# Kernel optimization log

Measured on AMD Instinct MI355X. Metric: run time of the kernel, lower is better.

The kernel has to match this reference:

```python
import jax, jax.numpy as jnp
import numpy as np
from jax import lax

# PRPN (Parse-Read-Predict Network), eval mode (all dropout off, BatchNorm in eval
# with running stats mean=0/var=1, rmask=ones). Submodule math follows the upstream
# yikangshen/PRPN implementation vendored by jiant: ParsingNetwork (conv gate stack,
# hard hardtanh memory gates with cumprod over slots), ReadingNetwork (masked-softmax
# attention over nslots memory + LayerNorm LSTM cell, shift-append memory update),
# PredictNetwork (attention over prediction memory, res=0 -> Linear+BN+Tanh head).

T, B, V, D, H, S, L, NL = 192, 32, 50000, 384, 384, 15, 5, 2
RES = 0.1
G4 = 4 * H
BN_SC = np.float32(1.0 / np.sqrt(1.0 + 1e-5))   # eval BatchNorm with mean=0, var=1
INV_SQRT_H = np.float32(1.0 / np.sqrt(H))


def _layer_norm(x, g, b, eps=1e-6):
    # torch-style LayerNorm with unbiased std (x.std(-1))
    mu = jnp.mean(x, -1, keepdims=True)
    var = jnp.sum((x - mu) ** 2, -1, keepdims=True) / (x.shape[-1] - 1)
    return g * (x - mu) / (jnp.sqrt(var) + eps) + b


def _msoftmax(logits, gate, eps=1e-8):
    # blocks.softmax: exp-normalize then multiply by (soft) gate mask before sum
    e = jnp.exp(logits - jnp.max(logits, -1, keepdims=True)) * gate
    return e / (jnp.sum(e, -1, keepdims=True) + eps)


def _forward(input_ids, emb_w, pconv1_w, pconv1_b, pbn_g, pbn_b, pconv2_w, pconv2_b,
             r_wih, r_bih, r_whh, r_bhh, r_lnih_g, r_lnih_b, r_lnhh_g, r_lnhh_b,
             r_lnc_g, r_lnc_b, r_proj_w, r_proj_b,
             p_proj_w, p_proj_b, p_ffd_w, p_ffd_b, p_bn_g, p_bn_b):
    emb = emb_w[input_ids]                                        # (T,B,D)

    # ---- ParsingNetwork ----
    x = jnp.concatenate([jnp.zeros((L, B, D), emb.dtype), emb], 0)  # (T+L,B,D), zero history
    xc = jnp.transpose(x, (1, 2, 0))                              # (B,D,T+L)
    h1 = lax.conv_general_dilated(xc, pconv1_w, (1,), 'VALID',
                                  dimension_numbers=('NCH', 'OIH', 'NCH'))
    h1 = h1 + pconv1_b[None, :, None]
    h1 = jax.nn.relu(pbn_g[None, :, None] * h1 * BN_SC + pbn_b[None, :, None])  # (B,H,T)
    half = H // 2
    # Conv1d(nhid, 2, 1, groups=2): channel 0 from first half, channel 1 from second
    gate = jax.nn.sigmoid(jnp.einsum('bct,c->bt', h1[:, :half], pconv2_w[0]) + pconv2_b[0])
    gate_next = jax.nn.sigmoid(jnp.einsum('bct,c->bt', h1[:, half:], pconv2_w[1]) + pconv2_b[1])
    cum = jnp.concatenate([jnp.full((B, S), 1e9, gate.dtype), gate], 1)  # init cum_gate = +inf
    gate_hat = jnp.stack([cum[:, S - k:S - k + T] for k in range(S)], 2)  # (B,T,S)

    def mem_gate(g):  # hard gates: (hardtanh((g-ghat)/res*2+1)+1)/2, cumprod over slots
        u = (jnp.clip((g[:, :, None] - gate_hat) / RES * 2.0 + 1.0, -1.0, 1.0) + 1.0) * 0.5
        return jnp.cumprod(u, axis=2)

    mg = jnp.transpose(mem_gate(gate), (1, 0, 2))                 # (T,B,S)
    mgn = jnp.transpose(mem_gate(gate_next), (1, 0, 2))           # (T,B,S)

    # ---- per-timestep Read / Predict-attention loop ----
    def step(carry, xs):
        mem_h, mem_c, pmem = carry       # (NL,B,S,H),(NL,B,S,H),(B,S,H)
        e_t, mg_t, mgn_t = xs
        h = e_t
        nh, nc = [], []
        for j in range(NL):
            mh, mc = mem_h[j], mem_c[j]
            key_j = jnp.concatenate([h, mh[:, -1]], -1) @ r_proj_w[j].T + r_proj_b[j]
            att = _msoftmax(jnp.einsum('bsh,bh->bs', mh, key_j) * INV_SQRT_H, mg_t)
            sel_h = jnp.einsum('bs,bsh->bh', att, mh)
            sel_c = jnp.einsum('bs,bsh->bh', att, mc)
            gates = (_layer_norm(h @ r_wih[j].T + r_bih[j], r_lnih_g[j], r_lnih_b[j])
                     + _layer_norm(sel_h @ r_whh[j].T + r_bhh[j], r_lnhh_g[j], r_lnhh_b[j]))
            i_g, f_g, c_g, o_g = jnp.split(gates, 4, axis=-1)
            c_new = jax.nn.sigmoid(f_g) * sel_c + jax.nn.sigmoid(i_g) * jnp.tanh(c_g)
            h_new = jax.nn.sigmoid(o_g) * jnp.tanh(_layer_norm(c_new, r_lnc_g[j], r_lnc_b[j]))
            nh.append(jnp.concatenate([mh[:, 1:], h_new[:, None]], 1))
            nc.append(jnp.concatenate([mc[:, 1:], c_new[:, None]], 1))
            h = h_new
        pkey = jnp.concatenate([h, pmem[:, -1]], -1) @ p_proj_w.T + p_proj_b
        patt = _msoftmax(jnp.einsum('bsh,bh->bs', pmem, pkey) * INV_SQRT_H, mgn_t)
        sel = jnp.einsum('bs,bsh->bh', patt, pmem)
        pmem_new = jnp.concatenate([pmem[:, 1:], h[:, None]], 1)
        return (jnp.stack(nh), jnp.stack(nc), pmem_new), (h, sel)

    carry0 = (jnp.zeros((NL, B, S, H), emb.dtype),
              jnp.zeros((NL, B, S, H), emb.dtype),
              jnp.zeros((B, S, H), emb.dtype))
    _, (out_h, out_sel) = lax.scan(step, carry0, (emb, mg, mgn))

    # ---- PredictNetwork head (res=0): Linear(2H->D) + BN(eval) + Tanh ----
    flat = jnp.concatenate([out_h.reshape(T * B, H), out_sel.reshape(T * B, H)], -1)
    y = flat @ p_ffd_w.T + p_ffd_b
    y = jnp.tanh(p_bn_g * y * BN_SC + p_bn_b)
    return y.reshape(T, B, D)


def setup_inputs() -> dict:
    key = jax.random.key(0)
    ks = iter(jax.random.split(key, 16))

    def rn(shape, s=0.05):
        return jax.random.normal(next(ks), shape, dtype=jnp.float32) * s

    return {
        "input_ids": jax.random.randint(next(ks), (T, B), 0, V),
        "emb_w": rn((V, D), 0.01),
        "pconv1_w": rn((H, D, L + 1)),
        "pconv1_b": jnp.zeros((H,), jnp.float32),
        "pbn_g": jnp.ones((H,), jnp.float32),
        "pbn_b": jnp.zeros((H,), jnp.float32),
        "pconv2_w": rn((2, H // 2)),
        "pconv2_b": jnp.zeros((2,), jnp.float32),
        "r_wih": rn((NL, G4, D)),
        "r_bih": jnp.zeros((NL, G4), jnp.float32),
        "r_whh": rn((NL, G4, H)),
        "r_bhh": jnp.zeros((NL, G4), jnp.float32),
        "r_lnih_g": jnp.ones((NL, G4), jnp.float32),
        "r_lnih_b": jnp.zeros((NL, G4), jnp.float32),
        "r_lnhh_g": jnp.ones((NL, G4), jnp.float32),
        "r_lnhh_b": jnp.zeros((NL, G4), jnp.float32),
        "r_lnc_g": jnp.ones((NL, H), jnp.float32),
        "r_lnc_b": jnp.zeros((NL, H), jnp.float32),
        "r_proj_w": rn((NL, H, D + H)),
        "r_proj_b": jnp.zeros((NL, H), jnp.float32),
        "p_proj_w": rn((H, 2 * H)),
        "p_proj_b": jnp.zeros((H,), jnp.float32),
        "p_ffd_w": rn((D, 2 * H)),
        "p_ffd_b": jnp.zeros((D,), jnp.float32),
        "p_bn_g": jnp.ones((D,), jnp.float32),
        "p_bn_b": jnp.zeros((D,), jnp.float32),
    }


def reference(input_ids, emb_w, pconv1_w, pconv1_b, pbn_g, pbn_b, pconv2_w, pconv2_b,
              r_wih, r_bih, r_whh, r_bhh, r_lnih_g, r_lnih_b, r_lnhh_g, r_lnhh_b,
              r_lnc_g, r_lnc_b, r_proj_w, r_proj_b,
              p_proj_w, p_proj_b, p_ffd_w, p_ffd_b, p_bn_g, p_bn_b):
    out = _forward(input_ids, emb_w, pconv1_w, pconv1_b, pbn_g, pbn_b, pconv2_w, pconv2_b,
                   r_wih, r_bih, r_whh, r_bhh, r_lnih_g, r_lnih_b, r_lnhh_g, r_lnhh_b,
                   r_lnc_g, r_lnc_b, r_proj_w, r_proj_b,
                   p_proj_w, p_proj_b, p_ffd_w, p_ffd_b, p_bn_g, p_bn_b)
    mask = input_ids != 0
    return out, mask
```

## Files before the change

kernel.cpp:

```cpp
#include <hip/hip_runtime.h>


#define TT 192
#define TB 6144

constexpr size_t O_EMB    = 0;
constexpr size_t O_IH0LN  = 2359296;
constexpr size_t O_KEY0E  = 11796480;
constexpr size_t O_MG     = 14155776;
constexpr size_t O_MGN    = 14247936;
constexpr size_t O_H1     = 14340096;
constexpr size_t O_P0S    = 14340096;
constexpr size_t O_P1S    = 14389248;
constexpr size_t O_IH1RAW = 14438400;
constexpr size_t O_KEY1H  = 14536704;
constexpr size_t O_KEY0MH = 14561280;
constexpr size_t O_KEY1MH = 14573568;
constexpr size_t O_PKEYH  = 14585856;
constexpr size_t O_PKEYMH = 14610432;
constexpr size_t O_HNEW0  = 14635008;
constexpr size_t O_HNEW1  = 14647296;
constexpr size_t O_BAR    = 14671872;
constexpr size_t O_DEADEND= 14672896;
constexpr size_t O_GATEA  = 16699392;
constexpr size_t O_GATEB  = 16705536;
constexpr size_t O_OUTHS  = 16711680;
constexpr size_t O_MEMH0  = 21430272;
constexpr size_t O_MEMC0  = 21614592;
constexpr size_t O_MEMH1  = 21798912;
constexpr size_t O_MEMC1  = 21983232;
constexpr size_t O_PMEM   = 22167552;
constexpr size_t O_P0     = 22351872;
constexpr size_t O_P1     = 23089152;
constexpr size_t O_STATEEND = 23826432;

#define A_GRP   0
#define A_ROOT  128
#define A_GEN   144
#define B_GRP   160
#define B_ROOT  272
#define B_GEN   288
#define PRCNT   304

__device__ __forceinline__ float sigmoidf(float x) { return 1.f / (1.f + expf(-x)); }

__device__ __forceinline__ float ldx(const float* p) {
  return __hip_atomic_load(p, __ATOMIC_RELAXED, __HIP_MEMORY_SCOPE_AGENT);
}
__device__ __forceinline__ void stx(float* p, float v) {
  __hip_atomic_store(p, v, __ATOMIC_RELAXED, __HIP_MEMORY_SCOPE_AGENT);
}
__device__ __forceinline__ float2 ldx2(const float* p) {
  unsigned long long v = __hip_atomic_load((const unsigned long long*)p,
                                           __ATOMIC_RELAXED, __HIP_MEMORY_SCOPE_AGENT);
  return __builtin_bit_cast(float2, v);
}
__device__ __forceinline__ void stx2(float* p, float2 v) {
  __hip_atomic_store((unsigned long long*)p, __builtin_bit_cast(unsigned long long, v),
                     __ATOMIC_RELAXED, __HIP_MEMORY_SCOPE_AGENT);
}
__device__ __forceinline__ unsigned ldu(const unsigned* p) {
  return __hip_atomic_load(p, __ATOMIC_RELAXED, __HIP_MEMORY_SCOPE_AGENT);
}

constexpr float BN_SC = 0.9999950000374997f;
constexpr float INV_SQRT_H = 0.05103103630798288f;

__device__ __forceinline__ float blockSum(float v, float* red) {
#pragma unroll
  for (int off = 32; off > 0; off >>= 1) v += __shfl_down(v, off, 64);
  __syncthreads();
  if ((threadIdx.x & 63) == 0) red[threadIdx.x >> 6] = v;
  __syncthreads();
  return red[0] + red[1] + red[2] + red[3];
}

__device__ __forceinline__ float2 blockSum2(float a, float b, float* red) {
#pragma unroll
  for (int off = 32; off > 0; off >>= 1) {
    a += __shfl_down(a, off, 64);
    b += __shfl_down(b, off, 64);
  }
  __syncthreads();
  if ((threadIdx.x & 63) == 0) { int w = threadIdx.x >> 6; red[2 * w] = a; red[2 * w + 1] = b; }
  __syncthreads();
  return make_float2(red[0] + red[2] + red[4] + red[6],
                     red[1] + red[3] + red[5] + red[7]);
}

__global__ __launch_bounds__(256) void k_zero(float* p, int n) {
  int i = blockIdx.x * 256 + threadIdx.x;
  int stride = gridDim.x * 256;
  for (; i < n; i += stride) p[i] = 0.f;
}

__global__ __launch_bounds__(256) void k_emb(const int* ids, const float* emb_w,
                                             float* emb, float* out) {
  size_t idx = (size_t)blockIdx.x * 256 + threadIdx.x;
  size_t stride = (size_t)gridDim.x * 256;
  for (size_t i = idx; i < (size_t)TB * 384; i += stride) {
    size_t tb = i / 384, d = i - tb * 384;
    int id = ids[tb];
    emb[i] = emb_w[(size_t)id * 384 + d];
    if (i < TB) out[(size_t)TB * 384 + i] = (ids[i] != 0) ? 1.f : 0.f;
  }
}

__global__ __launch_bounds__(256) void k_conv(const float* emb, const float* W1, const float* cbias,
                                              const float* bng, const float* bnb, float* h1) {
  __shared__ float As[32][68];
  __shared__ float Bs[32][68];
  int n0 = blockIdx.x * 64, m0 = blockIdx.y * 64;
  int tid = threadIdx.x;
  float acc[4][4] = {};
  int mi = tid >> 3, kq = tid & 7;
  int ni = tid >> 2, kb = tid & 3;
  for (int kk = 0; kk < 2304; kk += 32) {
    int kc = kk / 384, dbase = kk - kc * 384;
    __syncthreads();
#pragma unroll
    for (int p = 0; p < 2; ++p) {
      int m = m0 + mi + 32 * p;
      int b = m / 192, t = m - b * 192;
      int tt = t + kc - 5;
      float4 v = {0.f, 0.f, 0.f, 0.f};
      if (tt >= 0) v = *(const float4*)(emb + ((size_t)tt * 32 + b) * 384 + dbase + kq * 4);
      As[kq * 4 + 0][mi + 32 * p] = v.x; As[kq * 4 + 1][mi + 32 * p] = v.y;
      As[kq * 4 + 2][mi + 32 * p] = v.z; As[kq * 4 + 3][mi + 32 * p] = v.w;
    }
#pragma unroll
    for (int i = 0; i < 8; ++i) {
      int d = dbase + kb * 8 + i;
      Bs[kb * 8 + i][ni] = W1[(size_t)(n0 + ni) * 2304 + d * 6 + kc];
    }
    __syncthreads();
    int ty = tid >> 4, tx = tid & 15;
#pragma unroll
    for (int k = 0; k < 32; ++k) {
      float4 a = *(const float4*)(&As[k][ty * 4]);
      float4 bv = *(const float4*)(&Bs[k][tx * 4]);
      acc[0][0] += a.x * bv.x; acc[0][1] += a.x * bv.y; acc[0][2] += a.x * bv.z; acc[0][3] += a.x * bv.w;
      acc[1][0] += a.y * bv.x; acc[1][1] += a.y * bv.y; acc[1][2] += a.y * bv.z; acc[1][3] += a.y * bv.w;
      acc[2][0] += a.z * bv.x; acc[2][1] += a.z * bv.y; acc[2][2] += a.z * bv.z; acc[2][3] += a.z * bv.w;
      acc[3][0] += a.w * bv.x; acc[3][1] += a.w * bv.y; acc[3][2] += a.w * bv.z; acc[3][3] += a.w * bv.w;
    }
  }
  int ty = tid >> 4, tx = tid & 15;
#pragma unroll
  for (int i = 0; i < 4; ++i) {
    int m = m0 + ty * 4 + i;
#pragma unroll
    for (int j = 0; j < 4; ++j) {
      int n = n0 + tx * 4 + j;
      float v = acc[i][j] + cbias[n];
      v = bng[n] * v * BN_SC + bnb[n];
      h1[(size_t)m * 384 + n] = fmaxf(v, 0.f);
    }
  }
}

__global__ __launch_bounds__(256) void k_gate(const float* h1, const float* w2, const float* b2,
                                              float* gA, float* gB) {
  __shared__ float red[8];
  int bt = blockIdx.x, tid = threadIdx.x;
  float v0 = 0.f, v1 = 0.f;
  if (tid < 192) {
    v0 = h1[(size_t)bt * 384 + tid] * w2[tid];
    v1 = h1[(size_t)bt * 384 + 192 + tid] * w2[192 + tid];
  }
  float s0 = blockSum(v0, red);
  float s1 = blockSum(v1, red);
  if (tid == 0) {
    gA[bt] = 1.f / (1.f + expf(-(s0 + b2[0])));
    gB[bt] = 1.f / (1.f + expf(-(s1 + b2[1])));
  }
}

__global__ __launch_bounds__(256) void k_mg(const float* gA, const float* gB, float* mg, float* mgn) {
  int idx = blockIdx.x * 256 + threadIdx.x;
  if (idx >= TB) return;
  int t = idx >> 5, b = idx & 31;
  float g = gA[b * 192 + t], gn = gB[b * 192 + t];
  float p = 1.f, pn = 1.f;
  for (int k = 0; k < 15; ++k) {
    float ghat = (k <= t) ? gA[b * 192 + t - k] : 1e9f;
    float u = fminf(fmaxf((g - ghat) / 0.1f * 2.f + 1.f, -1.f), 1.f);
    float un = fminf(fmaxf((gn - ghat) / 0.1f * 2.f + 1.f, -1.f), 1.f);
    p *= (u + 1.f) * 0.5f;
    pn *= (un + 1.f) * 0.5f;
    mg[(size_t)idx * 15 + k] = p;
    mgn[(size_t)idx * 15 + k] = pn;
  }
}

__global__ __launch_bounds__(256) void k_gemm(const float* A, int lda, const float* W, int ldw,
                                              const float* bias, float* Cf, int ldc, int K, int mode,
                                              const float* bng, const float* bnb, float* Cb) {
  __shared__ float As[32][68];
  __shared__ float Bs[32][68];
  int n0 = blockIdx.x * 64, m0 = blockIdx.y * 64;
  int tid = threadIdx.x;
  float acc[4][4] = {};
  int mi = tid >> 3, kq = tid & 7;
  int ni = tid >> 2, kb = tid & 3;
  for (int kk = 0; kk < K; kk += 32) {
    __syncthreads();
#pragma unroll
    for (int p = 0; p < 2; ++p) {
      int m = m0 + mi + 32 * p;
      float4 v = *(const float4*)(A + (size_t)m * lda + kk + kq * 4);
      As[kq * 4 + 0][mi + 32 * p] = v.x; As[kq * 4 + 1][mi + 32 * p] = v.y;
      As[kq * 4 + 2][mi + 32 * p] = v.z; As[kq * 4 + 3][mi + 32 * p] = v.w;
    }
    {
      const float* wp = W + (size_t)(n0 + ni) * ldw + kk + kb * 8;
      float4 q0 = *(const float4*)(wp);
      float4 q1 = *(const float4*)(wp + 4);
      Bs[kb * 8 + 0][ni] = q0.x; Bs[kb * 8 + 1][ni] = q0.y;
      Bs[kb * 8 + 2][ni] = q0.z; Bs[kb * 8 + 3][ni] = q0.w;
      Bs[kb * 8 + 4][ni] = q1.x; Bs[kb * 8 + 5][ni] = q1.y;
      Bs[kb * 8 + 6][ni] = q1.z; Bs[kb * 8 + 7][ni] = q1.w;
    }
    __syncthreads();
    int ty = tid >> 4, tx = tid & 15;
#pragma unroll
    for (int k = 0; k < 32; ++k) {
      float4 a = *(const float4*)(&As[k][ty * 4]);
      float4 bv = *(const float4*)(&Bs[k][tx * 4]);
      acc[0][0] += a.x * bv.x; acc[0][1] += a.x * bv.y; acc[0][2] += a.x * bv.z; acc[0][3] += a.x * bv.w;
      acc[1][0] += a.y * bv.x; acc[1][1] += a.y * bv.y; acc[1][2] += a.y * bv.z; acc[1][3] += a.y * bv.w;
      acc[2][0] += a.z * bv.x; acc[2][1] += a.z * bv.y; acc[2][2] += a.z * bv.z; acc[2][3] += a.z * bv.w;
      acc[3][0] += a.w * bv.x; acc[3][1] += a.w * bv.y; acc[3][2] += a.w * bv.z; acc[3][3] += a.w * bv.w;
    }
  }
  int ty = tid >> 4, tx = tid & 15;
#pragma unroll
  for (int i = 0; i < 4; ++i) {
    int m = m0 + ty * 4 + i;
#pragma unroll
    for (int j = 0; j < 4; ++j) {
      int n = n0 + tx * 4 + j;
      float v = acc[i][j];
      if (bias) v += bias[n];
      if (mode == 0) Cf[(size_t)m * ldc + n] = v;
      else Cb[(size_t)m * ldc + n] = tanhf(bng[n] * v * BN_SC + bnb[n]);
    }
  }
}

__global__ __launch_bounds__(256) void k_ln_rows(float* X, const float* g, const float* bt) {
  __shared__ float red[8];
  float* x = X + (size_t)blockIdx.x * 1536;
  int tid = threadIdx.x;
  float ps = 0.f;
  for (int i = tid; i < 1536; i += 256) ps += x[i];
  float mu = blockSum(ps, red) * (1.f / 1536.f);
  ps = 0.f;
  for (int i = tid; i < 1536; i += 256) { float d = x[i] - mu; ps += d * d; }
  float inv = 1.f / (sqrtf(blockSum(ps, red) * (1.f / 1535.f)) + 1e-6f);
  for (int i = tid; i < 1536; i += 256) x[i] = g[i] * (x[i] - mu) * inv + bt[i];
}

struct ScanArgs {
  float* ws;
  const float *r_whh, *r_bhh, *r_lnhh_g, *r_lnhh_b, *r_lnih_g, *r_lnih_b;
  const float *r_lnc_g, *r_lnc_b, *r_wih, *r_bih, *r_proj_w, *r_proj_b;
  const float *p_proj_w, *p_proj_b;
};

struct GJob { const float* W; int ldw; int koff; const float* bias; float* dst; int rstride; int ncols; };

__device__ __forceinline__ void resolveJob(const GJob* J, int col, const float*& W, int& ldw, int& koff,
                                           const float*& bias, float*& dst, int& rstride, int& cc) {
  int c = col;
#pragma unroll
  for (int j = 0; j < 4; ++j) {
    if (c < J[j].ncols) {
      W = J[j].W; ldw = J[j].ldw; koff = J[j].koff; bias = J[j].bias;
      dst = J[j].dst; rstride = J[j].rstride; cc = c; return;
    }
    c -= J[j].ncols;
  }
  W = J[0].W; ldw = J[0].ldw; koff = J[0].koff; bias = J[0].bias;
  dst = J[0].dst; rstride = J[0].rstride; cc = 0;
}

__device__ __forceinline__ void gate_arrive(unsigned* bar, int grpBase, int rootOff,
                                            int genOff, int g, int ngroups, unsigned k) {
  unsigned a = __hip_atomic_fetch_add(bar + grpBase + g * 16, 1u, __ATOMIC_RELAXED, __HIP_MEMORY_SCOPE_AGENT);
  if (a == k * 16u + 15u) {
    unsigned r = __hip_atomic_fetch_add(bar + rootOff, 1u, __ATOMIC_RELAXED, __HIP_MEMORY_SCOPE_AGENT);
    if (r == k * (unsigned)ngroups + (unsigned)(ngroups - 1))
      __hip_atomic_store(bar + genOff, k + 1u, __ATOMIC_RELAXED, __HIP_MEMORY_SCOPE_AGENT);
  }
}
__device__ __forceinline__ void waitgen(const unsigned* bar, int genOff, unsigned tgt) {
  while (ldu(bar + genOff) < tgt) __builtin_amdgcn_s_sleep(2);
}

__device__ __forceinline__ void stage_x(const float* src, float* xs) {
  const int tid = threadIdx.x;
  for (int j2 = tid; j2 < 6144; j2 += 256) {
    int j = j2 * 2;
    int bb = j / 384, kk = j - bb * 384;
    float2 v = ldx2(src + j);
    xs[bb * 385 + kk] = v.x; xs[bb * 385 + kk + 1] = v.y;
  }
}

__device__ void gemv_run(const GJob* J, int cbase, int ncols, const float* xs, float* red) {
  const int tid = threadIdx.x;
  const int b = tid & 31, cg = tid >> 5;
  float xr[48];
  const float* xp = xs + b * 385 + cg * 48;
#pragma unroll
  for (int q = 0; q < 48; ++q) xr[q] = xp[q];
  for (int ch = 0; ch < ncols; ch += 21) {
    const int nch = min(21, ncols - ch);
    for (int ci = 0; ci < nch; ++ci) {
      const float* W; int ldw, koff; const float* bias; float* dst; int rstride; int cc;
      resolveJob(J, cbase + ch + ci, W, ldw, koff, bias, dst, rstride, cc);
      const float* wr = W + (size_t)cc * ldw + koff + cg * 48;
      float a = 0.f;
#pragma unroll
      for (int q = 0; q < 12; ++q) {
        float4 w = *(const float4*)(wr + q * 4);
        a += w.x * xr[q * 4 + 0] + w.y * xr[q * 4 + 1]
           + w.z * xr[q * 4 + 2] + w.w * xr[q * 4 + 3];
      }
      a += __shfl_down(a, 32, 64);
      if ((cg & 1) == 0) red[((cg >> 1) * nch + ci) * 33 + b] = a;
    }
    __syncthreads();
    const int pairs = nch * 32;
    for (int pi = tid; pi < pairs; pi += 256) {
      int bb = pi / nch, ci = pi - bb * nch;
      float s = red[(0 * nch + ci) * 33 + bb] + red[(1 * nch + ci) * 33 + bb]
              + red[(2 * nch + ci) * 33 + bb] + red[(3 * nch + ci) * 33 + bb];
      const float* W; int ldw, koff; const float* bias; float* dst; int rstride; int cc;
      resolveJob(J, cbase + ch + ci, W, ldw, koff, bias, dst, rstride, cc);
      if (bias) s += bias[cc];
      stx(dst + (size_t)bb * rstride + cc, s);
    }
    __syncthreads();
  }
}

__device__ void preload_l0(int t, int b, const ScanArgs& A, float* sm) {
  float* ws = A.ws;
  const int tid = threadIdx.x;
  const size_t tb = (size_t)t * 32 + b;
  float* keyl = sm; float* gih = sm + 1984;
  for (int n = tid; n < 1536; n += 256) gih[n] = ws[O_IH0LN + tb * 1536 + n];
  if (tid < 192) {
    float2 v = *(const float2*)(ws + O_KEY0E + tb * 384 + 2 * tid);
    keyl[2 * tid] = v.x; keyl[2 * tid + 1] = v.y;
  }
}

__device__ void per_b_attn(int t, const float* memh, float* sm, const float* mgp) {
  const int tid = threadIdx.x;
  float* keyl = sm; float* logit = sm + 384; float* att = sm + 400;
  float mgv = (tid < 15) ? mgp[tid] : 0.f;
  __syncthreads();
  {
    int s = tid >> 4, l = tid & 15;
    if (s < 15) {
      const float* mh = memh + ((t + s) % 15) * 384;
      float p = 0.f;
      for (int k = l; k < 384; k += 16) p += mh[k] * keyl[k];
      p += __shfl_down(p, 8, 64); p += __shfl_down(p, 4, 64);
      p += __shfl_down(p, 2, 64); p += __shfl_down(p, 1, 64);
      if (l == 0) logit[s] = p * INV_SQRT_H;
    }
  }
  __syncthreads();
  if (tid < 64) {
    float lg = (tid < 15) ? logit[tid] : -3.0e38f;
    lg = fmaxf(lg, __shfl_xor(lg, 8, 64));
    lg = fmaxf(lg, __shfl_xor(lg, 4, 64));
    lg = fmaxf(lg, __shfl_xor(lg, 2, 64));
    lg = fmaxf(lg, __shfl_xor(lg, 1, 64));
    float e = (tid < 15) ? expf(logit[tid] - lg) * mgv : 0.f;
    float ssum = e;
    ssum += __shfl_xor(ssum, 1, 64); ssum += __shfl_xor(ssum, 2, 64);
    ssum += __shfl_xor(ssum, 4, 64); ssum += __shfl_xor(ssum, 8, 64);
    if (tid < 15) att[tid] = e / (ssum + 1e-8f);
  }
  __syncthreads();
}

__device__ void per_b_tail(int layer, int t, int b, const ScanArgs& A, float* sm,
                           float* memh, float* memc, const float* mir,
                           float mu_ih, float inv_ih) {
  float* ws = A.ws;
  const int tid = threadIdx.x;
  const size_t tb = (size_t)t * 32 + b;
  float* att = sm + 400; float* red = sm + 416;
  float* ghh = sm + 448; float* gih = sm + 1984; float* selc = sm + 3520;
  float* cnew = sm + 3904; float* ogat = sm + 4288;
  float av[15]; int pidx[15];
#pragma unroll
  for (int i = 0; i < 15; ++i) { av[i] = att[i]; pidx[i] = (t + i) % 15; }
  const float* bhh = A.r_bhh + layer * 1536;
  for (int n = tid; n < 1536; n += 256) {
    float acc = bhh[n];
#pragma unroll
    for (int i = 0; i < 15; ++i) acc += av[i] * mir[(size_t)pidx[i] * 1536 + n];
    ghh[n] = acc;
  }
  for (int h = tid; h < 384; h += 256) {
    float acc = 0.f;
#pragma unroll
    for (int i = 0; i < 15; ++i) acc += av[i] * memc[pidx[i] * 384 + h];
    selc[h] = acc;
  }
  __syncthreads();
  float s1 = 0.f, s2 = 0.f;
  for (int n = tid; n < 1536; n += 256) { float v = ghh[n]; s1 += v; s2 += v * v; }
  float2 rhh = blockSum2(s1, s2, red);
  float mu_hh = rhh.x * (1.f / 1536.f);
  float inv_hh = 1.f / (sqrtf(fmaxf(rhh.y - rhh.x * mu_hh, 0.f) * (1.f / 1535.f)) + 1e-6f);
  const float *hg = A.r_lnhh_g + layer * 1536, *hb = A.r_lnhh_b + layer * 1536;
  const float *ig = A.r_lnih_g + 1536, *ib = A.r_lnih_b + 1536;
  for (int h = tid; h < 384; h += 256) {
    float gi, gf, gc, go;
    if (layer == 0) {
      gi = gih[h]; gf = gih[384 + h]; gc = gih[768 + h]; go = gih[1152 + h];
    } else {
      gi = ig[h] * (gih[h] - mu_ih) * inv_ih + ib[h];
      gf = ig[384 + h] * (gih[384 + h] - mu_ih) * inv_ih + ib[384 + h];
      gc = ig[768 + h] * (gih[768 + h] - mu_ih) * inv_ih + ib[768 + h];
      go = ig[1152 + h] * (gih[1152 + h] - mu_ih) * inv_ih + ib[1152 + h];
    }
    gi += hg[h] * (ghh[h] - mu_hh) * inv_hh + hb[h];
    gf += hg[384 + h] * (ghh[384 + h] - mu_hh) * inv_hh + hb[384 + h];
    gc += hg[768 + h] * (ghh[768 + h] - mu_hh) * inv_hh + hb[768 + h];
    go += hg[1152 + h] * (ghh[1152 + h] - mu_hh) * inv_hh + hb[1152 + h];
    float c = sigmoidf(gf) * selc[h] + sigmoidf(gi) * tanhf(gc);
    cnew[h] = c; ogat[h] = go;
  }
  __syncthreads();
  s1 = 0.f; s2 = 0.f;
  for (int h = tid; h < 384; h += 256) { float v = cnew[h]; s1 += v; s2 += v * v; }
  float2 rc = blockSum2(s1, s2, red);
  float mu_c = rc.x * (1.f / 384.f);
  float inv_c = 1.f / (sqrtf(fmaxf(rc.y - rc.x * mu_c, 0.f) * (1.f / 383.f)) + 1e-6f);
  const float *lcg = A.r_lnc_g + layer * 384, *lcb = A.r_lnc_b + layer * 384;
  const int slot = t % 15;
  if (tid < 192) {
    int h0 = 2 * tid, h1 = h0 + 1;
    float c0 = cnew[h0], c1 = cnew[h1];
    float hn0 = sigmoidf(ogat[h0]) * tanhf(lcg[h0] * (c0 - mu_c) * inv_c + lcb[h0]);
    float hn1 = sigmoidf(ogat[h1]) * tanhf(lcg[h1] * (c1 - mu_c) * inv_c + lcb[h1]);
    *(float2*)(memh + slot * 384 + h0) = make_float2(hn0, hn1);
    *(float2*)(memc + slot * 384 + h0) = make_float2(c0, c1);
    if (layer == 0) {
      stx2(ws + O_HNEW0 + (size_t)b * 384 + h0, make_float2(hn0, hn1));
    } else {
      stx2(ws + O_HNEW1 + (size_t)(t & 1) * 12288 + (size_t)b * 384 + h0, make_float2(hn0, hn1));
      *(float2*)(ws + O_OUTHS + tb * 768 + h0) = make_float2(hn0, hn1);
    }
  }
}

__device__ void per_b_layer0(int t, int b, const ScanArgs& A, float* sm) {
  float* ws = A.ws;
  const int tid = threadIdx.x;
  const size_t tb = (size_t)t * 32 + b;
  float* memh = ws + O_MEMH0 + (size_t)b * 5760;
  float* memc = ws + O_MEMC0 + (size_t)b * 5760;
  float* mir  = ws + O_P0 + (size_t)b * 23040;
  const float* stg = ws + O_P0S + (size_t)b * 1536;
  float* keyl = sm;
  const int pslot = (t + 14) % 15;
#pragma unroll
  for (int i = 0; i < 3; ++i) {
    int idx = tid + i * 256;
    float2 v = ldx2(stg + 2 * idx);
    *(float2*)(mir + (size_t)pslot * 1536 + 2 * idx) = v;
  }
  if (tid < 192) {
    float2 c = ldx2(ws + O_KEY0MH + (size_t)b * 384 + 2 * tid);
    keyl[2 * tid] += c.x; keyl[2 * tid + 1] += c.y;
  }
  per_b_attn(t, memh, sm, ws + O_MG + tb * 15);
  per_b_tail(0, t, b, A, sm, memh, memc, mir, 0.f, 0.f);
}

__device__ void per_b_layer1(int t, int b, const ScanArgs& A, float* sm) {
  float* ws = A.ws;
  const int tid = threadIdx.x;
  const size_t tb = (size_t)t * 32 + b;
  const size_t par = (size_t)(t & 1);
  float* memh = ws + O_MEMH1 + (size_t)b * 5760;
  float* memc = ws + O_MEMC1 + (size_t)b * 5760;
  float* mir  = ws + O_P1 + (size_t)b * 23040;
  const float* stg = ws + O_P1S + (size_t)b * 1536;
  float* keyl = sm; float* red = sm + 416; float* gih = sm + 1984;
  const int pslot = (t + 14) % 15;
#pragma unroll
  for (int i = 0; i < 3; ++i) {
    int idx = tid + i * 256;
    float2 v = ldx2(stg + 2 * idx);
    *(float2*)(mir + (size_t)pslot * 1536 + 2 * idx) = v;
  }
#pragma unroll
  for (int i = 0; i < 3; ++i) {
    int idx = tid + i * 256;
    float2 v = ldx2(ws + O_IH1RAW + par * 49152 + (size_t)b * 1536 + 2 * idx);
    gih[2 * idx] = v.x; gih[2 * idx + 1] = v.y;
  }
  if (tid < 192) {
    float2 a = ldx2(ws + O_KEY1H + par * 12288 + (size_t)b * 384 + 2 * tid);
    float2 c = ldx2(ws + O_KEY1MH + (size_t)b * 384 + 2 * tid);
    keyl[2 * tid] = a.x + c.x; keyl[2 * tid + 1] = a.y + c.y;
  }
  per_b_attn(t, memh, sm, ws + O_MG + tb * 15);
  float s1 = 0.f, s2 = 0.f;
  for (int n = tid; n < 1536; n += 256) { float v = gih[n]; s1 += v; s2 += v * v; }
  float2 rih = blockSum2(s1, s2, red);
  float mu_ih = rih.x * (1.f / 1536.f);
  float inv_ih = 1.f / (sqrtf(fmaxf(rih.y - rih.x * mu_ih, 0.f) * (1.f / 1535.f)) + 1e-6f);
  per_b_tail(1, t, b, A, sm, memh, memc, mir, mu_ih, inv_ih);
}

__device__ void per_b_predict(int t, int b, const ScanArgs& A, float* sm) {
  float* ws = A.ws;
  const int tid = threadIdx.x;
  const size_t tb = (size_t)t * 32 + b;
  float* pmem = ws + O_PMEM + (size_t)b * 5760;
  float* keyl = sm; float* logit = sm + 384; float* att = sm + 400;
  if (tid < 192) {
    float2 a = ldx2(ws + O_PKEYH + (size_t)(t & 1) * 12288 + (size_t)b * 384 + 2 * tid);
    float2 c = ldx2(ws + O_PKEYMH + (size_t)((t + 1) & 1) * 12288 + (size_t)b * 384 + 2 * tid);
    keyl[2 * tid] = a.x + c.x; keyl[2 * tid + 1] = a.y + c.y;
  }
  float mgv = (tid < 15) ? ws[O_MGN + tb * 15 + tid] : 0.f;
  __syncthreads();
  {
    int s = tid >> 4, l = tid & 15;
    if (s < 15) {
      const float* mh = pmem + ((t + s) % 15) * 384;
      float p = 0.f;
      for (int k = l; k < 384; k += 16) p += mh[k] * keyl[k];
      p += __shfl_down(p, 8, 64); p += __shfl_down(p, 4, 64);
      p += __shfl_down(p, 2, 64); p += __shfl_down(p, 1, 64);
      if (l == 0) logit[s] = p * INV_SQRT_H;
    }
  }
  __syncthreads();
  if (tid < 64) {
    float lg = (tid < 15) ? logit[tid] : -3.0e38f;
    lg = fmaxf(lg, __shfl_xor(lg, 8, 64));
    lg = fmaxf(lg, __shfl_xor(lg, 4, 64));
    lg = fmaxf(lg, __shfl_xor(lg, 2, 64));
    lg = fmaxf(lg, __shfl_xor(lg, 1, 64));
    float e = (tid < 15) ? expf(logit[tid] - lg) * mgv : 0.f;
    float ssum = e;
    ssum += __shfl_xor(ssum, 1, 64); ssum += __shfl_xor(ssum, 2, 64);
    ssum += __shfl_xor(ssum, 4, 64); ssum += __shfl_xor(ssum, 8, 64);
    if (tid < 15) att[tid] = e / (ssum + 1e-8f);
  }
  __syncthreads();
  float av[15]; int pidx[15];
#pragma unroll
  for (int i = 0; i < 15; ++i) { av[i] = att[i]; pidx[i] = (t + i) % 15; }
  for (int h = tid; h < 384; h += 256) {
    float acc = 0.f;
#pragma unroll
    for (int i = 0; i < 15; ++i) acc += av[i] * pmem[pidx[i] * 384 + h];
    ws[O_OUTHS + tb * 768 + 384 + h] = acc;
  }
  __syncthreads();
  if (tid < 192) {
    const int slot = t % 15;
    float2 v = ldx2(ws + O_HNEW1 + (size_t)(t & 1) * 12288 + (size_t)b * 384 + 2 * tid);
    *(float2*)(pmem + slot * 384 + 2 * tid) = v;
  }
}

__global__ __launch_bounds__(256) void k_scan(ScanArgs A) {
  __shared__ float sm[15104];
  float* ws = A.ws;
  unsigned* bar = (unsigned*)(ws + O_BAR);
  const int wg = blockIdx.x;
  const int tid = threadIdx.x;

  if (wg < 32) {
    const int b = wg, g = wg >> 4;
    preload_l0(0, b, A, sm);
    __syncthreads();
    unsigned ka = 0;
    for (int t = 0; t < 192; ++t, ka += 2) {
      per_b_layer0(t, b, A, sm);
      __syncthreads();
      if (tid == 0) gate_arrive(bar, A_GRP, A_ROOT, A_GEN, g, 8, ka);
      if (t + 1 < 192) preload_l0(t + 1, b, A, sm);
      __syncthreads();
      if (tid == 0) {
        waitgen(bar, A_GEN, ka + 1);
        gate_arrive(bar, A_GRP, A_ROOT, A_GEN, g, 8, ka + 1);
        waitgen(bar, A_GEN, ka + 2);
      }
      __syncthreads();
    }
  } else if (wg < 128) {
    const int g = wg >> 4;
    const int cbase = (wg - 32) * 40;
    float* xs = sm; float* red = sm + 12320;
    unsigned ka = 0;
    for (int t = 0; t < 192; ++t, ka += 2) {
      if (tid == 0) {
        gate_arrive(bar, A_GRP, A_ROOT, A_GEN, g, 8, ka);
        waitgen(bar, A_GEN, ka + 1);
      }
      __syncthreads();
      stage_x(ws + O_HNEW0, xs);
      if (tid == 0 && t >= 2) waitgen(bar, B_GEN, 2u * t - 3u);
      __syncthreads();
      {
        const size_t par = (size_t)(t & 1);
        GJob J[4] = {
          { A.r_wih + 589824, 384, 0, A.r_bih + 1536, ws + O_IH1RAW + par * 49152, 1536, 1536 },
          { A.r_proj_w + 294912, 768, 0, A.r_proj_b + 384, ws + O_KEY1H + par * 12288, 384, 384 },
          { A.r_whh, 384, 0, nullptr, ws + O_P0S, 1536, 1536 },
          { A.r_proj_w, 768, 384, nullptr, ws + O_KEY0MH, 384, 384 },
        };
        gemv_run(J, cbase, 40, xs, red);
      }
      if (tid == 0) {
        gate_arrive(bar, A_GRP, A_ROOT, A_GEN, g, 8, ka + 1);
        waitgen(bar, A_GEN, ka + 2);
      }
      __syncthreads();
    }
  } else if (wg < 160) {
    const int b = wg - 128, g = (wg - 128) >> 4;
    unsigned kb = 0;
    for (int t = 0; t < 192; ++t, kb += 2) {
      if (tid == 0) waitgen(bar, A_GEN, 2u * t + 2u);
      __syncthreads();
      per_b_layer1(t, b, A, sm);
      __syncthreads();
      if (tid == 0) {
        gate_arrive(bar, B_GRP, B_ROOT, B_GEN, g, 6, kb);
        waitgen(bar, B_GEN, kb + 1);
        gate_arrive(bar, B_GRP, B_ROOT, B_GEN, g, 6, kb + 1);
        waitgen(bar, B_GEN, kb + 2);
      }
      __syncthreads();
    }
  } else if (wg < 224) {
    const int g = (wg - 128) >> 4;
    const int cbase = (wg - 160) * 42;
    float* xs = sm; float* red = sm + 12320;
    unsigned kb = 0;
    for (int t = 0; t < 192; ++t, kb += 2) {
      if (tid == 0) {
        gate_arrive(bar, B_GRP, B_ROOT, B_GEN, g, 6, kb);
        waitgen(bar, B_GEN, kb + 1);
      }
      __syncthreads();
      stage_x(ws + O_HNEW1 + (size_t)(t & 1) * 12288, xs);
      if (tid == 0) {
        while (ldu(bar + PRCNT) < 32u * (unsigned)t) __builtin_amdgcn_s_sleep(2);
      }
      __syncthreads();
      {
        const size_t par = (size_t)(t & 1);
        GJob J[4] = {
          { A.r_whh + 589824, 384, 0, nullptr, ws + O_P1S, 1536, 1536 },
          { A.r_proj_w + 294912, 768, 384, nullptr, ws + O_KEY1MH, 384, 384 },
          { A.p_proj_w, 768, 0, A.p_proj_b, ws + O_PKEYH + par * 12288, 384, 384 },
          { A.p_proj_w, 768, 384, nullptr, ws + O_PKEYMH + par * 12288, 384, 384 },
        };
        gemv_run(J, cbase, 42, xs, red);
      }
      if (tid == 0) {
        gate_arrive(bar, B_GRP, B_ROOT, B_GEN, g, 6, kb + 1);
        waitgen(bar, B_GEN, kb + 2);
      }
      __syncthreads();
    }
  } else {
    const int b = wg - 224;
    for (int t = 0; t < 192; ++t) {
      if (tid == 0) waitgen(bar, B_GEN, 2u * t + 2u);
      __syncthreads();
      per_b_predict(t, b, A, sm);
      __syncthreads();
      if (tid == 0)
        __hip_atomic_fetch_add(bar + PRCNT, 1u, __ATOMIC_RELAXED, __HIP_MEMORY_SCOPE_AGENT);
    }
  }
}

extern "C" void kernel_launch(void* const* d_in, const int* in_sizes, int n_in,
                              void* d_out, int out_size, void* d_ws, size_t ws_size,
                              hipStream_t stream) {
  const int* ids = (const int*)d_in[0];
  const float* emb_w = (const float*)d_in[1];
  const float* pconv1_w = (const float*)d_in[2];
  const float* pconv1_b = (const float*)d_in[3];
  const float* pbn_g = (const float*)d_in[4];
  const float* pbn_b = (const float*)d_in[5];
  const float* pconv2_w = (const float*)d_in[6];
  const float* pconv2_b = (const float*)d_in[7];
  const float* r_wih = (const float*)d_in[8];
  const float* r_bih = (const float*)d_in[9];
  const float* r_whh = (const float*)d_in[10];
  const float* r_bhh = (const float*)d_in[11];
  const float* r_lnih_g = (const float*)d_in[12];
  const float* r_lnih_b = (const float*)d_in[13];
  const float* r_lnhh_g = (const float*)d_in[14];
  const float* r_lnhh_b = (const float*)d_in[15];
  const float* r_lnc_g = (const float*)d_in[16];
  const float* r_lnc_b = (const float*)d_in[17];
  const float* r_proj_w = (const float*)d_in[18];
  const float* r_proj_b = (const float*)d_in[19];
  const float* p_proj_w = (const float*)d_in[20];
  const float* p_proj_b = (const float*)d_in[21];
  const float* p_ffd_w = (const float*)d_in[22];
  const float* p_ffd_b = (const float*)d_in[23];
  const float* p_bn_g = (const float*)d_in[24];
  const float* p_bn_b = (const float*)d_in[25];
  float* ws = (float*)d_ws;
  float* out = (float*)d_out;

  k_zero<<<1024, 256, 0, stream>>>(ws + O_MEMH0, (int)(O_STATEEND - O_MEMH0));
  k_emb<<<4096, 256, 0, stream>>>(ids, emb_w, ws + O_EMB, out);
  k_conv<<<dim3(6, 96), 256, 0, stream>>>(ws + O_EMB, pconv1_w, pconv1_b, pbn_g, pbn_b, ws + O_H1);
  k_gate<<<6144, 256, 0, stream>>>(ws + O_H1, pconv2_w, pconv2_b, ws + O_GATEA, ws + O_GATEB);
  k_mg<<<24, 256, 0, stream>>>(ws + O_GATEA, ws + O_GATEB, ws + O_MG, ws + O_MGN);
  k_zero<<<326, 256, 0, stream>>>(ws + O_P0S, (int)(O_DEADEND - O_P0S));
  k_gemm<<<dim3(24, 96), 256, 0, stream>>>(ws + O_EMB, 384, r_wih, 384, r_bih,
                                           ws + O_IH0LN, 1536, 384, 0, nullptr, nullptr, nullptr);
  k_gemm<<<dim3(6, 96), 256, 0, stream>>>(ws + O_EMB, 384, r_proj_w, 768, r_proj_b,
                                          ws + O_KEY0E, 384, 384, 0, nullptr, nullptr, nullptr);
  k_ln_rows<<<6144, 256, 0, stream>>>(ws + O_IH0LN, r_lnih_g, r_lnih_b);
  ScanArgs SA{ws, r_whh, r_bhh, r_lnhh_g, r_lnhh_b, r_lnih_g, r_lnih_b,
              r_lnc_g, r_lnc_b, r_wih, r_bih, r_proj_w, r_proj_b, p_proj_w, p_proj_b};
  k_scan<<<256, 256, 0, stream>>>(SA);
  k_gemm<<<dim3(6, 96), 256, 0, stream>>>(ws + O_OUTHS, 768, p_ffd_w, 768, p_ffd_b,
                                          nullptr, 384, 768, 1, p_bn_g, p_bn_b, out);
}
```

Before: 13.15 ms.

## Replace grouped barriers with per-block progress flags and wave-per-batch recurrent cells

The persistent scan kernel's hierarchical generation barriers give way to per-workgroup monotonic progress flags. Each consumer polls only the producers it depends on, so layer 0, layer 1, predict and the GEMV groups can run skewed in a pipeline instead of in lockstep. The per-batch cell work (attention, LayerNorm-LSTM, predict) moves from a full 256-thread block per batch element to one wave per batch element, using register-resident data and wave shuffles instead of block-wide syncs. The grid shrinks from 256 to 184 blocks. The risks are subtle ordering bugs under relaxed atomics and lower parallelism per batch step.

```diff
diff --git a/kernel.cpp b/kernel.cpp
--- a/kernel.cpp
+++ b/kernel.cpp
@@ -21,7 +21,7 @@
 constexpr size_t O_HNEW0  = 14635008;
 constexpr size_t O_HNEW1  = 14647296;
 constexpr size_t O_BAR    = 14671872;
-constexpr size_t O_DEADEND= 14672896;
+constexpr size_t O_DEADEND= 14675968;
 constexpr size_t O_GATEA  = 16699392;
 constexpr size_t O_GATEB  = 16705536;
 constexpr size_t O_OUTHS  = 16711680;
@@ -34,13 +34,11 @@
 constexpr size_t O_P1     = 23089152;
 constexpr size_t O_STATEEND = 23826432;
 
-#define A_GRP   0
-#define A_ROOT  128
-#define A_GEN   144
-#define B_GRP   160
-#define B_ROOT  272
-#define B_GEN   288
-#define PRCNT   304
+#define L0F 0
+#define L1F 512
+#define PRF 1024
+#define G0F 1536
+#define G1F 3072
 
 __device__ __forceinline__ float sigmoidf(float x) { return 1.f / (1.f + expf(-x)); }
 
@@ -59,8 +57,11 @@
   __hip_atomic_store((unsigned long long*)p, __builtin_bit_cast(unsigned long long, v),
                      __ATOMIC_RELAXED, __HIP_MEMORY_SCOPE_AGENT);
 }
-__device__ __forceinline__ unsigned ldu(const unsigned* p) {
+__device__ __forceinline__ int ldi(const int* p) {
   return __hip_atomic_load(p, __ATOMIC_RELAXED, __HIP_MEMORY_SCOPE_AGENT);
+}
+__device__ __forceinline__ void sti(int* p, int v) {
+  __hip_atomic_store(p, v, __ATOMIC_RELAXED, __HIP_MEMORY_SCOPE_AGENT);
 }
 
 constexpr float BN_SC = 0.9999950000374997f;
@@ -75,17 +76,13 @@
   return red[0] + red[1] + red[2] + red[3];
 }
 
-__device__ __forceinline__ float2 blockSum2(float a, float b, float* red) {
+__device__ __forceinline__ float2 wred2(float a, float b) {
 #pragma unroll
   for (int off = 32; off > 0; off >>= 1) {
-    a += __shfl_down(a, off, 64);
-    b += __shfl_down(b, off, 64);
-  }
-  __syncthreads();
-  if ((threadIdx.x & 63) == 0) { int w = threadIdx.x >> 6; red[2 * w] = a; red[2 * w + 1] = b; }
-  __syncthreads();
-  return make_float2(red[0] + red[2] + red[4] + red[6],
-                     red[1] + red[3] + red[5] + red[7]);
+    a += __shfl_xor(a, off, 64);
+    b += __shfl_xor(b, off, 64);
+  }
+  return make_float2(a, b);
 }
 
 __global__ __launch_bounds__(256) void k_zero(float* p, int n) {
@@ -285,19 +282,6 @@
   dst = J[0].dst; rstride = J[0].rstride; cc = 0;
 }
 
-__device__ __forceinline__ void gate_arrive(unsigned* bar, int grpBase, int rootOff,
-                                            int genOff, int g, int ngroups, unsigned k) {
-  unsigned a = __hip_atomic_fetch_add(bar + grpBase + g * 16, 1u, __ATOMIC_RELAXED, __HIP_MEMORY_SCOPE_AGENT);
-  if (a == k * 16u + 15u) {
-    unsigned r = __hip_atomic_fetch_add(bar + rootOff, 1u, __ATOMIC_RELAXED, __HIP_MEMORY_SCOPE_AGENT);
-    if (r == k * (unsigned)ngroups + (unsigned)(ngroups - 1))
-      __hip_atomic_store(bar + genOff, k + 1u, __ATOMIC_RELAXED, __HIP_MEMORY_SCOPE_AGENT);
-  }
-}
-__device__ __forceinline__ void waitgen(const unsigned* bar, int genOff, unsigned tgt) {
-  while (ldu(bar + genOff) < tgt) __builtin_amdgcn_s_sleep(2);
-}
-
 __device__ __forceinline__ void stage_x(const float* src, float* xs) {
   const int tid = threadIdx.x;
   for (int j2 = tid; j2 < 6144; j2 += 256) {
@@ -346,354 +330,418 @@
   }
 }
 
-__device__ void preload_l0(int t, int b, const ScanArgs& A, float* sm) {
+__device__ __forceinline__ void wave_attn(const float* memh, const float* klds, const float* mgp,
+                                          int t, int lane, float (&att)[15]) {
+  const int g = lane >> 2, l = lane & 3;
+  float part = 0.f;
+  if (g < 15) {
+    const float* mh = memh + ((t + g) % 15) * 384 + l;
+#pragma unroll 8
+    for (int k = 0; k < 96; ++k) part += mh[4 * k] * klds[l + 4 * k];
+  }
+  part += __shfl_xor(part, 1, 64);
+  part += __shfl_xor(part, 2, 64);
+  float logit[15];
+#pragma unroll
+  for (int s = 0; s < 15; ++s) logit[s] = __shfl(part, 4 * s, 64) * INV_SQRT_H;
+  float m = logit[0];
+#pragma unroll
+  for (int s = 1; s < 15; ++s) m = fmaxf(m, logit[s]);
+  float sum = 0.f;
+#pragma unroll
+  for (int s = 0; s < 15; ++s) { att[s] = expf(logit[s] - m) * mgp[s]; sum += att[s]; }
+  float inv = 1.f / (sum + 1e-8f);
+#pragma unroll
+  for (int s = 0; s < 15; ++s) att[s] *= inv;
+}
+
+__device__ void l0_loop(int b, int lane, float* klds, const ScanArgs& A, int* bar) {
   float* ws = A.ws;
-  const int tid = threadIdx.x;
-  const size_t tb = (size_t)t * 32 + b;
-  float* keyl = sm; float* gih = sm + 1984;
-  for (int n = tid; n < 1536; n += 256) gih[n] = ws[O_IH0LN + tb * 1536 + n];
-  if (tid < 192) {
-    float2 v = *(const float2*)(ws + O_KEY0E + tb * 384 + 2 * tid);
-    keyl[2 * tid] = v.x; keyl[2 * tid + 1] = v.y;
-  }
-}
-
-__device__ void per_b_attn(int t, const float* memh, float* sm, const float* mgp) {
-  const int tid = threadIdx.x;
-  float* keyl = sm; float* logit = sm + 384; float* att = sm + 400;
-  float mgv = (tid < 15) ? mgp[tid] : 0.f;
-  __syncthreads();
-  {
-    int s = tid >> 4, l = tid & 15;
-    if (s < 15) {
-      const float* mh = memh + ((t + s) % 15) * 384;
-      float p = 0.f;
-      for (int k = l; k < 384; k += 16) p += mh[k] * keyl[k];
-      p += __shfl_down(p, 8, 64); p += __shfl_down(p, 4, 64);
-      p += __shfl_down(p, 2, 64); p += __shfl_down(p, 1, 64);
-      if (l == 0) logit[s] = p * INV_SQRT_H;
-    }
-  }
-  __syncthreads();
-  if (tid < 64) {
-    float lg = (tid < 15) ? logit[tid] : -3.0e38f;
-    lg = fmaxf(lg, __shfl_xor(lg, 8, 64));
-    lg = fmaxf(lg, __shfl_xor(lg, 4, 64));
-    lg = fmaxf(lg, __shfl_xor(lg, 2, 64));
-    lg = fmaxf(lg, __shfl_xor(lg, 1, 64));
-    float e = (tid < 15) ? expf(logit[tid] - lg) * mgv : 0.f;
-    float ssum = e;
-    ssum += __shfl_xor(ssum, 1, 64); ssum += __shfl_xor(ssum, 2, 64);
-    ssum += __shfl_xor(ssum, 4, 64); ssum += __shfl_xor(ssum, 8, 64);
-    if (tid < 15) att[tid] = e / (ssum + 1e-8f);
-  }
-  __syncthreads();
-}
-
-__device__ void per_b_tail(int layer, int t, int b, const ScanArgs& A, float* sm,
-                           float* memh, float* memc, const float* mir,
-                           float mu_ih, float inv_ih) {
-  float* ws = A.ws;
-  const int tid = threadIdx.x;
-  const size_t tb = (size_t)t * 32 + b;
-  float* att = sm + 400; float* red = sm + 416;
-  float* ghh = sm + 448; float* gih = sm + 1984; float* selc = sm + 3520;
-  float* cnew = sm + 3904; float* ogat = sm + 4288;
-  float av[15]; int pidx[15];
-#pragma unroll
-  for (int i = 0; i < 15; ++i) { av[i] = att[i]; pidx[i] = (t + i) % 15; }
-  const float* bhh = A.r_bhh + layer * 1536;
-  for (int n = tid; n < 1536; n += 256) {
-    float acc = bhh[n];
-#pragma unroll
-    for (int i = 0; i < 15; ++i) acc += av[i] * mir[(size_t)pidx[i] * 1536 + n];
-    ghh[n] = acc;
-  }
-  for (int h = tid; h < 384; h += 256) {
-    float acc = 0.f;
-#pragma unroll
-    for (int i = 0; i < 15; ++i) acc += av[i] * memc[pidx[i] * 384 + h];
-    selc[h] = acc;
-  }
-  __syncthreads();
-  float s1 = 0.f, s2 = 0.f;
-  for (int n = tid; n < 1536; n += 256) { float v = ghh[n]; s1 += v; s2 += v * v; }
-  float2 rhh = blockSum2(s1, s2, red);
-  float mu_hh = rhh.x * (1.f / 1536.f);
-  float inv_hh = 1.f / (sqrtf(fmaxf(rhh.y - rhh.x * mu_hh, 0.f) * (1.f / 1535.f)) + 1e-6f);
-  const float *hg = A.r_lnhh_g + layer * 1536, *hb = A.r_lnhh_b + layer * 1536;
-  const float *ig = A.r_lnih_g + 1536, *ib = A.r_lnih_b + 1536;
-  for (int h = tid; h < 384; h += 256) {
-    float gi, gf, gc, go;
-    if (layer == 0) {
-      gi = gih[h]; gf = gih[384 + h]; gc = gih[768 + h]; go = gih[1152 + h];
-    } else {
-      gi = ig[h] * (gih[h] - mu_ih) * inv_ih + ib[h];
-      gf = ig[384 + h] * (gih[384 + h] - mu_ih) * inv_ih + ib[384 + h];
-      gc = ig[768 + h] * (gih[768 + h] - mu_ih) * inv_ih + ib[768 + h];
-      go = ig[1152 + h] * (gih[1152 + h] - mu_ih) * inv_ih + ib[1152 + h];
-    }
-    gi += hg[h] * (ghh[h] - mu_hh) * inv_hh + hb[h];
-    gf += hg[384 + h] * (ghh[384 + h] - mu_hh) * inv_hh + hb[384 + h];
-    gc += hg[768 + h] * (ghh[768 + h] - mu_hh) * inv_hh + hb[768 + h];
-    go += hg[1152 + h] * (ghh[1152 + h] - mu_hh) * inv_hh + hb[1152 + h];
-    float c = sigmoidf(gf) * selc[h] + sigmoidf(gi) * tanhf(gc);
-    cnew[h] = c; ogat[h] = go;
-  }
-  __syncthreads();
-  s1 = 0.f; s2 = 0.f;
-  for (int h = tid; h < 384; h += 256) { float v = cnew[h]; s1 += v; s2 += v * v; }
-  float2 rc = blockSum2(s1, s2, red);
-  float mu_c = rc.x * (1.f / 384.f);
-  float inv_c = 1.f / (sqrtf(fmaxf(rc.y - rc.x * mu_c, 0.f) * (1.f / 383.f)) + 1e-6f);
-  const float *lcg = A.r_lnc_g + layer * 384, *lcb = A.r_lnc_b + layer * 384;
-  const int slot = t % 15;
-  if (tid < 192) {
-    int h0 = 2 * tid, h1 = h0 + 1;
-    float c0 = cnew[h0], c1 = cnew[h1];
-    float hn0 = sigmoidf(ogat[h0]) * tanhf(lcg[h0] * (c0 - mu_c) * inv_c + lcb[h0]);
-    float hn1 = sigmoidf(ogat[h1]) * tanhf(lcg[h1] * (c1 - mu_c) * inv_c + lcb[h1]);
-    *(float2*)(memh + slot * 384 + h0) = make_float2(hn0, hn1);
-    *(float2*)(memc + slot * 384 + h0) = make_float2(c0, c1);
-    if (layer == 0) {
-      stx2(ws + O_HNEW0 + (size_t)b * 384 + h0, make_float2(hn0, hn1));
-    } else {
-      stx2(ws + O_HNEW1 + (size_t)(t & 1) * 12288 + (size_t)b * 384 + h0, make_float2(hn0, hn1));
-      *(float2*)(ws + O_OUTHS + tb * 768 + h0) = make_float2(hn0, hn1);
-    }
-  }
-}
-
-__device__ void per_b_layer0(int t, int b, const ScanArgs& A, float* sm) {
-  float* ws = A.ws;
-  const int tid = threadIdx.x;
-  const size_t tb = (size_t)t * 32 + b;
   float* memh = ws + O_MEMH0 + (size_t)b * 5760;
   float* memc = ws + O_MEMC0 + (size_t)b * 5760;
   float* mir  = ws + O_P0 + (size_t)b * 23040;
   const float* stg = ws + O_P0S + (size_t)b * 1536;
-  float* keyl = sm;
-  const int pslot = (t + 14) % 15;
-#pragma unroll
-  for (int i = 0; i < 3; ++i) {
-    int idx = tid + i * 256;
-    float2 v = ldx2(stg + 2 * idx);
-    *(float2*)(mir + (size_t)pslot * 1536 + 2 * idx) = v;
-  }
-  if (tid < 192) {
-    float2 c = ldx2(ws + O_KEY0MH + (size_t)b * 384 + 2 * tid);
-    keyl[2 * tid] += c.x; keyl[2 * tid + 1] += c.y;
-  }
-  per_b_attn(t, memh, sm, ws + O_MG + tb * 15);
-  per_b_tail(0, t, b, A, sm, memh, memc, mir, 0.f, 0.f);
-}
-
-__device__ void per_b_layer1(int t, int b, const ScanArgs& A, float* sm) {
+  const int* p1 = bar + G0F + lane * 16;
+  const int* p2 = bar + G0F + (64 + (lane & 31)) * 16;
+  for (int t = 0; t < 192; ++t) {
+    const size_t tb = (size_t)t * 32 + b;
+    float2 ih[12];
+#pragma unroll
+    for (int j = 0; j < 12; ++j)
+      ih[j] = *(const float2*)(ws + O_IH0LN + tb * 1536 + 2 * lane + 128 * j);
+    float2 kE[3];
+#pragma unroll
+    for (int j = 0; j < 3; ++j)
+      kE[j] = *(const float2*)(ws + O_KEY0E + tb * 384 + 2 * lane + 128 * j);
+    while (true) {
+      int a = ldi(p1);
+      int c = (lane < 32) ? ldi(p2) : 0x7fffffff;
+      if (__all(a >= t && c >= t)) break;
+      __builtin_amdgcn_s_sleep(1);
+    }
+    float2 fresh[12];
+#pragma unroll
+    for (int j = 0; j < 12; ++j) fresh[j] = ldx2(stg + 2 * lane + 128 * j);
+#pragma unroll
+    for (int j = 0; j < 3; ++j) {
+      float2 c2 = ldx2(ws + O_KEY0MH + (size_t)b * 384 + 2 * lane + 128 * j);
+      *(float2*)(klds + 2 * lane + 128 * j) = make_float2(kE[j].x + c2.x, kE[j].y + c2.y);
+    }
+    float att[15];
+    wave_attn(memh, klds, ws + O_MG + tb * 15, t, lane, att);
+    float2 acc[12];
+#pragma unroll
+    for (int j = 0; j < 12; ++j) {
+      float2 bb = *(const float2*)(A.r_bhh + 2 * lane + 128 * j);
+      acc[j] = make_float2(bb.x + att[14] * fresh[j].x, bb.y + att[14] * fresh[j].y);
+    }
+#pragma unroll
+    for (int s = 0; s < 14; ++s) {
+      const float* P = mir + ((t + s) % 15) * 1536;
+      float a = att[s];
+#pragma unroll
+      for (int j = 0; j < 12; ++j) {
+        float2 p = *(const float2*)(P + 2 * lane + 128 * j);
+        acc[j].x += a * p.x; acc[j].y += a * p.y;
+      }
+    }
+    float2 selc[3];
+#pragma unroll
+    for (int j = 0; j < 3; ++j) selc[j] = make_float2(0.f, 0.f);
+#pragma unroll
+    for (int s = 0; s < 15; ++s) {
+      const float* C = memc + ((t + s) % 15) * 384;
+      float a = att[s];
+#pragma unroll
+      for (int j = 0; j < 3; ++j) {
+        float2 p = *(const float2*)(C + 2 * lane + 128 * j);
+        selc[j].x += a * p.x; selc[j].y += a * p.y;
+      }
+    }
+    float s1 = 0.f, s2 = 0.f;
+#pragma unroll
+    for (int j = 0; j < 12; ++j) {
+      s1 += acc[j].x + acc[j].y;
+      s2 += acc[j].x * acc[j].x + acc[j].y * acc[j].y;
+    }
+    float2 r = wred2(s1, s2);
+    float mu = r.x * (1.f / 1536.f);
+    float inv = 1.f / (sqrtf(fmaxf(r.y - r.x * mu, 0.f) * (1.f / 1535.f)) + 1e-6f);
+    const float* hg = A.r_lnhh_g;
+    const float* hb = A.r_lnhh_b;
+    float2 cn[3], og[3];
+#pragma unroll
+    for (int jj = 0; jj < 3; ++jj) {
+      const int d = 2 * lane + 128 * jj;
+      float2 gi, gf, gc, go;
+      { float2 g2 = *(const float2*)(hg + d), b2 = *(const float2*)(hb + d);
+        gi.x = ih[jj].x + g2.x * (acc[jj].x - mu) * inv + b2.x;
+        gi.y = ih[jj].y + g2.y * (acc[jj].y - mu) * inv + b2.y; }
+      { float2 g2 = *(const float2*)(hg + 384 + d), b2 = *(const float2*)(hb + 384 + d);
+        gf.x = ih[3 + jj].x + g2.x * (acc[3 + jj].x - mu) * inv + b2.x;
+        gf.y = ih[3 + jj].y + g2.y * (acc[3 + jj].y - mu) * inv + b2.y; }
+      { float2 g2 = *(const float2*)(hg + 768 + d), b2 = *(const float2*)(hb + 768 + d);
+        gc.x = ih[6 + jj].x + g2.x * (acc[6 + jj].x - mu) * inv + b2.x;
+        gc.y = ih[6 + jj].y + g2.y * (acc[6 + jj].y - mu) * inv + b2.y; }
+      { float2 g2 = *(const float2*)(hg + 1152 + d), b2 = *(const float2*)(hb + 1152 + d);
+        go.x = ih[9 + jj].x + g2.x * (acc[9 + jj].x - mu) * inv + b2.x;
+        go.y = ih[9 + jj].y + g2.y * (acc[9 + jj].y - mu) * inv + b2.y; }
+      cn[jj].x = sigmoidf(gf.x) * selc[jj].x + sigmoidf(gi.x) * tanhf(gc.x);
+      cn[jj].y = sigmoidf(gf.y) * selc[jj].y + sigmoidf(gi.y) * tanhf(gc.y);
+      og[jj] = go;
+    }
+    s1 = 0.f; s2 = 0.f;
+#pragma unroll
+    for (int jj = 0; jj < 3; ++jj) {
+      s1 += cn[jj].x + cn[jj].y;
+      s2 += cn[jj].x * cn[jj].x + cn[jj].y * cn[jj].y;
+    }
+    r = wred2(s1, s2);
+    float mu_c = r.x * (1.f / 384.f);
+    float inv_c = 1.f / (sqrtf(fmaxf(r.y - r.x * mu_c, 0.f) * (1.f / 383.f)) + 1e-6f);
+    const int slot = t % 15;
+    const int pslot = (t + 14) % 15;
+#pragma unroll
+    for (int jj = 0; jj < 3; ++jj) {
+      const int d = 2 * lane + 128 * jj;
+      float2 lg2 = *(const float2*)(A.r_lnc_g + d), lb2 = *(const float2*)(A.r_lnc_b + d);
+      float2 hn;
+      hn.x = sigmoidf(og[jj].x) * tanhf(lg2.x * (cn[jj].x - mu_c) * inv_c + lb2.x);
+      hn.y = sigmoidf(og[jj].y) * tanhf(lg2.y * (cn[jj].y - mu_c) * inv_c + lb2.y);
+      *(float2*)(memh + slot * 384 + d) = hn;
+      *(float2*)(memc + slot * 384 + d) = cn[jj];
+      stx2(ws + O_HNEW0 + (size_t)b * 384 + d, hn);
+    }
+#pragma unroll
+    for (int j = 0; j < 12; ++j)
+      *(float2*)(mir + pslot * 1536 + 2 * lane + 128 * j) = fresh[j];
+    asm volatile("s_waitcnt vmcnt(0)" ::: "memory");
+    if (lane == 0) sti(bar + L0F + b * 16, t + 1);
+  }
+}
+
+__device__ void l1_loop(int b, int lane, float* klds, const ScanArgs& A, int* bar) {
   float* ws = A.ws;
-  const int tid = threadIdx.x;
-  const size_t tb = (size_t)t * 32 + b;
-  const size_t par = (size_t)(t & 1);
   float* memh = ws + O_MEMH1 + (size_t)b * 5760;
   float* memc = ws + O_MEMC1 + (size_t)b * 5760;
   float* mir  = ws + O_P1 + (size_t)b * 23040;
   const float* stg = ws + O_P1S + (size_t)b * 1536;
-  float* keyl = sm; float* red = sm + 416; float* gih = sm + 1984;
-  const int pslot = (t + 14) % 15;
-#pragma unroll
-  for (int i = 0; i < 3; ++i) {
-    int idx = tid + i * 256;
-    float2 v = ldx2(stg + 2 * idx);
-    *(float2*)(mir + (size_t)pslot * 1536 + 2 * idx) = v;
-  }
-#pragma unroll
-  for (int i = 0; i < 3; ++i) {
-    int idx = tid + i * 256;
-    float2 v = ldx2(ws + O_IH1RAW + par * 49152 + (size_t)b * 1536 + 2 * idx);
-    gih[2 * idx] = v.x; gih[2 * idx + 1] = v.y;
-  }
-  if (tid < 192) {
-    float2 a = ldx2(ws + O_KEY1H + par * 12288 + (size_t)b * 384 + 2 * tid);
-    float2 c = ldx2(ws + O_KEY1MH + (size_t)b * 384 + 2 * tid);
-    keyl[2 * tid] = a.x + c.x; keyl[2 * tid + 1] = a.y + c.y;
-  }
-  per_b_attn(t, memh, sm, ws + O_MG + tb * 15);
-  float s1 = 0.f, s2 = 0.f;
-  for (int n = tid; n < 1536; n += 256) { float v = gih[n]; s1 += v; s2 += v * v; }
-  float2 rih = blockSum2(s1, s2, red);
-  float mu_ih = rih.x * (1.f / 1536.f);
-  float inv_ih = 1.f / (sqrtf(fmaxf(rih.y - rih.x * mu_ih, 0.f) * (1.f / 1535.f)) + 1e-6f);
-  per_b_tail(1, t, b, A, sm, memh, memc, mir, mu_ih, inv_ih);
-}
-
-__device__ void per_b_predict(int t, int b, const ScanArgs& A, float* sm) {
+  const float* hg = A.r_lnhh_g + 1536;
+  const float* hb = A.r_lnhh_b + 1536;
+  const float* igp = A.r_lnih_g + 1536;
+  const float* ibp = A.r_lnih_b + 1536;
+  const float* bhh = A.r_bhh + 1536;
+  const float* lcg = A.r_lnc_g + 384;
+  const float* lcb = A.r_lnc_b + 384;
+  const int* p1 = bar + G0F + lane * 16;
+  const int* p2 = bar + G0F + (64 + (lane & 31)) * 16;
+  const int* p3 = bar + G1F + lane * 16;
+  for (int t = 0; t < 192; ++t) {
+    while (true) {
+      int a = ldi(p1);
+      int c = (lane < 32) ? ldi(p2) : 0x7fffffff;
+      int d2 = ldi(p3);
+      if (__all(a >= t + 1 && c >= t + 1 && d2 >= t)) break;
+      __builtin_amdgcn_s_sleep(1);
+    }
+    const size_t tb = (size_t)t * 32 + b;
+    const size_t par = (size_t)(t & 1);
+    float2 gx[12], fresh[12];
+#pragma unroll
+    for (int j = 0; j < 12; ++j) {
+      gx[j] = ldx2(ws + O_IH1RAW + par * 49152 + (size_t)b * 1536 + 2 * lane + 128 * j);
+      fresh[j] = ldx2(stg + 2 * lane + 128 * j);
+    }
+#pragma unroll
+    for (int j = 0; j < 3; ++j) {
+      float2 a2 = ldx2(ws + O_KEY1H + par * 12288 + (size_t)b * 384 + 2 * lane + 128 * j);
+      float2 c2 = ldx2(ws + O_KEY1MH + (size_t)b * 384 + 2 * lane + 128 * j);
+      *(float2*)(klds + 2 * lane + 128 * j) = make_float2(a2.x + c2.x, a2.y + c2.y);
+    }
+    float att[15];
+    wave_attn(memh, klds, ws + O_MG + tb * 15, t, lane, att);
+    float2 acc[12];
+#pragma unroll
+    for (int j = 0; j < 12; ++j) {
+      float2 bb = *(const float2*)(bhh + 2 * lane + 128 * j);
+      acc[j] = make_float2(bb.x + att[14] * fresh[j].x, bb.y + att[14] * fresh[j].y);
+    }
+#pragma unroll
+    for (int s = 0; s < 14; ++s) {
+      const float* P = mir + ((t + s) % 15) * 1536;
+      float a = att[s];
+#pragma unroll
+      for (int j = 0; j < 12; ++j) {
+        float2 p = *(const float2*)(P + 2 * lane + 128 * j);
+        acc[j].x += a * p.x; acc[j].y += a * p.y;
+      }
+    }
+    float2 selc[3];
+#pragma unroll
+    for (int j = 0; j < 3; ++j) selc[j] = make_float2(0.f, 0.f);
+#pragma unroll
+    for (int s = 0; s < 15; ++s) {
+      const float* C = memc + ((t + s) % 15) * 384;
+      float a = att[s];
+#pragma unroll
+      for (int j = 0; j < 3; ++j) {
+        float2 p = *(const float2*)(C + 2 * lane + 128 * j);
+        selc[j].x += a * p.x; selc[j].y += a * p.y;
+      }
+    }
+    float s1 = 0.f, s2 = 0.f;
+#pragma unroll
+    for (int j = 0; j < 12; ++j) {
+      s1 += gx[j].x + gx[j].y;
+      s2 += gx[j].x * gx[j].x + gx[j].y * gx[j].y;
+    }
+    float2 r = wred2(s1, s2);
+    float mu_i = r.x * (1.f / 1536.f);
+    float inv_i = 1.f / (sqrtf(fmaxf(r.y - r.x * mu_i, 0.f) * (1.f / 1535.f)) + 1e-6f);
+    s1 = 0.f; s2 = 0.f;
+#pragma unroll
+    for (int j = 0; j < 12; ++j) {
+      s1 += acc[j].x + acc[j].y;
+      s2 += acc[j].x * acc[j].x + acc[j].y * acc[j].y;
+    }
+    r = wred2(s1, s2);
+    float mu = r.x * (1.f / 1536.f);
+    float inv = 1.f / (sqrtf(fmaxf(r.y - r.x * mu, 0.f) * (1.f / 1535.f)) + 1e-6f);
+    float2 cn[3], og[3];
+#pragma unroll
+    for (int jj = 0; jj < 3; ++jj) {
+      const int d = 2 * lane + 128 * jj;
+      float2 gi, gf, gc, go;
+      { float2 i2 = *(const float2*)(igp + d), ib2 = *(const float2*)(ibp + d);
+        float2 g2 = *(const float2*)(hg + d), b2 = *(const float2*)(hb + d);
+        gi.x = i2.x * (gx[jj].x - mu_i) * inv_i + ib2.x + g2.x * (acc[jj].x - mu) * inv + b2.x;
+        gi.y = i2.y * (gx[jj].y - mu_i) * inv_i + ib2.y + g2.y * (acc[jj].y - mu) * inv + b2.y; }
+      { float2 i2 = *(const float2*)(igp + 384 + d), ib2 = *(const float2*)(ibp + 384 + d);
+        float2 g2 = *(const float2*)(hg + 384 + d), b2 = *(const float2*)(hb + 384 + d);
+        gf.x = i2.x * (gx[3 + jj].x - mu_i) * inv_i + ib2.x + g2.x * (acc[3 + jj].x - mu) * inv + b2.x;
+        gf.y = i2.y * (gx[3 + jj].y - mu_i) * inv_i + ib2.y + g2.y * (acc[3 + jj].y - mu) * inv + b2.y; }
+      { float2 i2 = *(const float2*)(igp + 768 + d), ib2 = *(const float2*)(ibp + 768 + d);
+        float2 g2 = *(const float2*)(hg + 768 + d), b2 = *(const float2*)(hb + 768 + d);
+        gc.x = i2.x * (gx[6 + jj].x - mu_i) * inv_i + ib2.x + g2.x * (acc[6 + jj].x - mu) * inv + b2.x;
+        gc.y = i2.y * (gx[6 + jj].y - mu_i) * inv_i + ib2.y + g2.y * (acc[6 + jj].y - mu) * inv + b2.y; }
+      { float2 i2 = *(const float2*)(igp + 1152 + d), ib2 = *(const float2*)(ibp + 1152 + d);
+        float2 g2 = *(const float2*)(hg + 1152 + d), b2 = *(const float2*)(hb + 1152 + d);
+        go.x = i2.x * (gx[9 + jj].x - mu_i) * inv_i + ib2.x + g2.x * (acc[9 + jj].x - mu) * inv + b2.x;
+        go.y = i2.y * (gx[9 + jj].y - mu_i) * inv_i + ib2.y + g2.y * (acc[9 + jj].y - mu) * inv + b2.y; }
+      cn[jj].x = sigmoidf(gf.x) * selc[jj].x + sigmoidf(gi.x) * tanhf(gc.x);
+      cn[jj].y = sigmoidf(gf.y) * selc[jj].y + sigmoidf(gi.y) * tanhf(gc.y);
+      og[jj] = go;
+    }
+    s1 = 0.f; s2 = 0.f;
+#pragma unroll
+    for (int jj = 0; jj < 3; ++jj) {
+      s1 += cn[jj].x + cn[jj].y;
+      s2 += cn[jj].x * cn[jj].x + cn[jj].y * cn[jj].y;
+    }
+    r = wred2(s1, s2);
+    float mu_c = r.x * (1.f / 384.f);
+    float inv_c = 1.f / (sqrtf(fmaxf(r.y - r.x * mu_c, 0.f) * (1.f / 383.f)) + 1e-6f);
+    const int slot = t % 15;
+    const int pslot = (t + 14) % 15;
+#pragma unroll
+    for (int jj = 0; jj < 3; ++jj) {
+      const int d = 2 * lane + 128 * jj;
+      float2 lg2 = *(const float2*)(lcg + d), lb2 = *(const float2*)(lcb + d);
+      float2 hn;
+      hn.x = sigmoidf(og[jj].x) * tanhf(lg2.x * (cn[jj].x - mu_c) * inv_c + lb2.x);
+      hn.y = sigmoidf(og[jj].y) * tanhf(lg2.y * (cn[jj].y - mu_c) * inv_c + lb2.y);
+      *(float2*)(memh + slot * 384 + d) = hn;
+      *(float2*)(memc + slot * 384 + d) = cn[jj];
+      stx2(ws + O_HNEW1 + par * 12288 + (size_t)b * 384 + d, hn);
+      *(float2*)(ws + O_OUTHS + tb * 768 + d) = hn;
+    }
+#pragma unroll
+    for (int j = 0; j < 12; ++j)
+      *(float2*)(mir + pslot * 1536 + 2 * lane + 128 * j) = fresh[j];
+    asm volatile("s_waitcnt vmcnt(0)" ::: "memory");
+    if (lane == 0) sti(bar + L1F + b * 16, t + 1);
+  }
+}
+
+__device__ void pr_loop(int b, int lane, float* klds, const ScanArgs& A, int* bar) {
+  float* ws = A.ws;
+  float* pmem = ws + O_PMEM + (size_t)b * 5760;
+  const int* p1 = bar + G1F + lane * 16;
+  for (int t = 0; t < 192; ++t) {
+    while (true) {
+      int a = ldi(p1);
+      if (__all(a >= t + 1)) break;
+      __builtin_amdgcn_s_sleep(1);
+    }
+    const size_t tb = (size_t)t * 32 + b;
+#pragma unroll
+    for (int j = 0; j < 3; ++j) {
+      float2 a2 = ldx2(ws + O_PKEYH + (size_t)(t & 1) * 12288 + (size_t)b * 384 + 2 * lane + 128 * j);
+      float2 c2 = ldx2(ws + O_PKEYMH + (size_t)((t + 1) & 1) * 12288 + (size_t)b * 384 + 2 * lane + 128 * j);
+      *(float2*)(klds + 2 * lane + 128 * j) = make_float2(a2.x + c2.x, a2.y + c2.y);
+    }
+    float att[15];
+    wave_attn(pmem, klds, ws + O_MGN + tb * 15, t, lane, att);
+    float2 sel[3];
+#pragma unroll
+    for (int j = 0; j < 3; ++j) sel[j] = make_float2(0.f, 0.f);
+#pragma unroll
+    for (int s = 0; s < 15; ++s) {
+      const float* P = pmem + ((t + s) % 15) * 384;
+      float a = att[s];
+#pragma unroll
+      for (int j = 0; j < 3; ++j) {
+        float2 p = *(const float2*)(P + 2 * lane + 128 * j);
+        sel[j].x += a * p.x; sel[j].y += a * p.y;
+      }
+    }
+#pragma unroll
+    for (int j = 0; j < 3; ++j)
+      *(float2*)(ws + O_OUTHS + tb * 768 + 384 + 2 * lane + 128 * j) = sel[j];
+#pragma unroll
+    for (int j = 0; j < 3; ++j) {
+      float2 v = ldx2(ws + O_HNEW1 + (size_t)(t & 1) * 12288 + (size_t)b * 384 + 2 * lane + 128 * j);
+      *(float2*)(pmem + (t % 15) * 384 + 2 * lane + 128 * j) = v;
+    }
+    asm volatile("s_waitcnt vmcnt(0)" ::: "memory");
+    if (lane == 0) sti(bar + PRF + b * 16, t + 1);
+  }
+}
+
+__device__ void g0_loop(int gwg, const ScanArgs& A, int* bar, float* sm) {
   float* ws = A.ws;
   const int tid = threadIdx.x;
-  const size_t tb = (size_t)t * 32 + b;
-  float* pmem = ws + O_PMEM + (size_t)b * 5760;
-  float* keyl = sm; float* logit = sm + 384; float* att = sm + 400;
-  if (tid < 192) {
-    float2 a = ldx2(ws + O_PKEYH + (size_t)(t & 1) * 12288 + (size_t)b * 384 + 2 * tid);
-    float2 c = ldx2(ws + O_PKEYMH + (size_t)((t + 1) & 1) * 12288 + (size_t)b * 384 + 2 * tid);
-    keyl[2 * tid] = a.x + c.x; keyl[2 * tid + 1] = a.y + c.y;
-  }
-  float mgv = (tid < 15) ? ws[O_MGN + tb * 15 + tid] : 0.f;
-  __syncthreads();
-  {
-    int s = tid >> 4, l = tid & 15;
-    if (s < 15) {
-      const float* mh = pmem + ((t + s) % 15) * 384;
-      float p = 0.f;
-      for (int k = l; k < 384; k += 16) p += mh[k] * keyl[k];
-      p += __shfl_down(p, 8, 64); p += __shfl_down(p, 4, 64);
-      p += __shfl_down(p, 2, 64); p += __shfl_down(p, 1, 64);
-      if (l == 0) logit[s] = p * INV_SQRT_H;
-    }
-  }
-  __syncthreads();
-  if (tid < 64) {
-    float lg = (tid < 15) ? logit[tid] : -3.0e38f;
-    lg = fmaxf(lg, __shfl_xor(lg, 8, 64));
-    lg = fmaxf(lg, __shfl_xor(lg, 4, 64));
-    lg = fmaxf(lg, __shfl_xor(lg, 2, 64));
-    lg = fmaxf(lg, __shfl_xor(lg, 1, 64));
-    float e = (tid < 15) ? expf(logit[tid] - lg) * mgv : 0.f;
-    float ssum = e;
-    ssum += __shfl_xor(ssum, 1, 64); ssum += __shfl_xor(ssum, 2, 64);
-    ssum += __shfl_xor(ssum, 4, 64); ssum += __shfl_xor(ssum, 8, 64);
-    if (tid < 15) att[tid] = e / (ssum + 1e-8f);
-  }
-  __syncthreads();
-  float av[15]; int pidx[15];
-#pragma unroll
-  for (int i = 0; i < 15; ++i) { av[i] = att[i]; pidx[i] = (t + i) % 15; }
-  for (int h = tid; h < 384; h += 256) {
-    float acc = 0.f;
-#pragma unroll
-    for (int i = 0; i < 15; ++i) acc += av[i] * pmem[pidx[i] * 384 + h];
-    ws[O_OUTHS + tb * 768 + 384 + h] = acc;
-  }
-  __syncthreads();
-  if (tid < 192) {
-    const int slot = t % 15;
-    float2 v = ldx2(ws + O_HNEW1 + (size_t)(t & 1) * 12288 + (size_t)b * 384 + 2 * tid);
-    *(float2*)(pmem + slot * 384 + 2 * tid) = v;
+  float* xs = sm;
+  float* red = sm + 12320;
+  const int cbase = gwg * 40;
+  for (int t = 0; t < 192; ++t) {
+    if (tid < 64) {
+      const int* p = (tid < 32) ? (bar + L0F + tid * 16) : (bar + L1F + (tid - 32) * 16);
+      const int tgt = (tid < 32) ? (t + 1) : (t - 1);
+      while (true) {
+        int v = ldi(p);
+        if (__all(v >= tgt)) break;
+        __builtin_amdgcn_s_sleep(1);
+      }
+    }
+    __syncthreads();
+    stage_x(ws + O_HNEW0, xs);
+    __syncthreads();
+    const size_t par = (size_t)(t & 1);
+    GJob J[4] = {
+      { A.r_wih + 589824, 384, 0, A.r_bih + 1536, ws + O_IH1RAW + par * 49152, 1536, 1536 },
+      { A.r_proj_w + 294912, 768, 0, A.r_proj_b + 384, ws + O_KEY1H + par * 12288, 384, 384 },
+      { A.r_whh, 384, 0, nullptr, ws + O_P0S, 1536, 1536 },
+      { A.r_proj_w, 768, 384, nullptr, ws + O_KEY0MH, 384, 384 },
+    };
+    gemv_run(J, cbase, 40, xs, red);
+    if (tid == 0) sti(bar + G0F + gwg * 16, t + 1);
+  }
+}
+
+__device__ void g1_loop(int gwg, const ScanArgs& A, int* bar, float* sm) {
+  float* ws = A.ws;
+  const int tid = threadIdx.x;
+  float* xs = sm;
+  float* red = sm + 12320;
+  const int cbase = gwg * 42;
+  for (int t = 0; t < 192; ++t) {
+    if (tid < 64) {
+      const int* p = (tid < 32) ? (bar + L1F + tid * 16) : (bar + PRF + (tid - 32) * 16);
+      const int tgt = (tid < 32) ? (t + 1) : t;
+      while (true) {
+        int v = ldi(p);
+        if (__all(v >= tgt)) break;
+        __builtin_amdgcn_s_sleep(1);
+      }
+    }
+    __syncthreads();
+    const size_t par = (size_t)(t & 1);
+    stage_x(ws + O_HNEW1 + par * 12288, xs);
+    __syncthreads();
+    GJob J[4] = {
+      { A.r_whh + 589824, 384, 0, nullptr, ws + O_P1S, 1536, 1536 },
+      { A.r_proj_w + 294912, 768, 384, nullptr, ws + O_KEY1MH, 384, 384 },
+      { A.p_proj_w, 768, 0, A.p_proj_b, ws + O_PKEYH + par * 12288, 384, 384 },
+      { A.p_proj_w, 768, 384, nullptr, ws + O_PKEYMH + par * 12288, 384, 384 },
+    };
+    gemv_run(J, cbase, 42, xs, red);
+    if (tid == 0) sti(bar + G1F + gwg * 16, t + 1);
   }
 }
 
 __global__ __launch_bounds__(256) void k_scan(ScanArgs A) {
   __shared__ float sm[15104];
-  float* ws = A.ws;
-  unsigned* bar = (unsigned*)(ws + O_BAR);
+  int* bar = (int*)(A.ws + O_BAR);
   const int wg = blockIdx.x;
   const int tid = threadIdx.x;
-
-  if (wg < 32) {
-    const int b = wg, g = wg >> 4;
-    preload_l0(0, b, A, sm);
-    __syncthreads();
-    unsigned ka = 0;
-    for (int t = 0; t < 192; ++t, ka += 2) {
-      per_b_layer0(t, b, A, sm);
-      __syncthreads();
-      if (tid == 0) gate_arrive(bar, A_GRP, A_ROOT, A_GEN, g, 8, ka);
-      if (t + 1 < 192) preload_l0(t + 1, b, A, sm);
-      __syncthreads();
-      if (tid == 0) {
-        waitgen(bar, A_GEN, ka + 1);
-        gate_arrive(bar, A_GRP, A_ROOT, A_GEN, g, 8, ka + 1);
-        waitgen(bar, A_GEN, ka + 2);
-      }
-      __syncthreads();
-    }
-  } else if (wg < 128) {
-    const int g = wg >> 4;
-    const int cbase = (wg - 32) * 40;
-    float* xs = sm; float* red = sm + 12320;
-    unsigned ka = 0;
-    for (int t = 0; t < 192; ++t, ka += 2) {
-      if (tid == 0) {
-        gate_arrive(bar, A_GRP, A_ROOT, A_GEN, g, 8, ka);
-        waitgen(bar, A_GEN, ka + 1);
-      }
-      __syncthreads();
-      stage_x(ws + O_HNEW0, xs);
-      if (tid == 0 && t >= 2) waitgen(bar, B_GEN, 2u * t - 3u);
-      __syncthreads();
-      {
-        const size_t par = (size_t)(t & 1);
-        GJob J[4] = {
-          { A.r_wih + 589824, 384, 0, A.r_bih + 1536, ws + O_IH1RAW + par * 49152, 1536, 1536 },
-          { A.r_proj_w + 294912, 768, 0, A.r_proj_b + 384, ws + O_KEY1H + par * 12288, 384, 384 },
-          { A.r_whh, 384, 0, nullptr, ws + O_P0S, 1536, 1536 },
-          { A.r_proj_w, 768, 384, nullptr, ws + O_KEY0MH, 384, 384 },
-        };
-        gemv_run(J, cbase, 40, xs, red);
-      }
-      if (tid == 0) {
-        gate_arrive(bar, A_GRP, A_ROOT, A_GEN, g, 8, ka + 1);
-        waitgen(bar, A_GEN, ka + 2);
-      }
-      __syncthreads();
-    }
-  } else if (wg < 160) {
-    const int b = wg - 128, g = (wg - 128) >> 4;
-    unsigned kb = 0;
-    for (int t = 0; t < 192; ++t, kb += 2) {
-      if (tid == 0) waitgen(bar, A_GEN, 2u * t + 2u);
-      __syncthreads();
-      per_b_layer1(t, b, A, sm);
-      __syncthreads();
-      if (tid == 0) {
-        gate_arrive(bar, B_GRP, B_ROOT, B_GEN, g, 6, kb);
-        waitgen(bar, B_GEN, kb + 1);
-        gate_arrive(bar, B_GRP, B_ROOT, B_GEN, g, 6, kb + 1);
-        waitgen(bar, B_GEN, kb + 2);
-      }
-      __syncthreads();
-    }
-  } else if (wg < 224) {
-    const int g = (wg - 128) >> 4;
-    const int cbase = (wg - 160) * 42;
-    float* xs = sm; float* red = sm + 12320;
-    unsigned kb = 0;
-    for (int t = 0; t < 192; ++t, kb += 2) {
-      if (tid == 0) {
-        gate_arrive(bar, B_GRP, B_ROOT, B_GEN, g, 6, kb);
-        waitgen(bar, B_GEN, kb + 1);
-      }
-      __syncthreads();
-      stage_x(ws + O_HNEW1 + (size_t)(t & 1) * 12288, xs);
-      if (tid == 0) {
-        while (ldu(bar + PRCNT) < 32u * (unsigned)t) __builtin_amdgcn_s_sleep(2);
-      }
-      __syncthreads();
-      {
-        const size_t par = (size_t)(t & 1);
-        GJob J[4] = {
-          { A.r_whh + 589824, 384, 0, nullptr, ws + O_P1S, 1536, 1536 },
-          { A.r_proj_w + 294912, 768, 384, nullptr, ws + O_KEY1MH, 384, 384 },
-          { A.p_proj_w, 768, 0, A.p_proj_b, ws + O_PKEYH + par * 12288, 384, 384 },
-          { A.p_proj_w, 768, 384, nullptr, ws + O_PKEYMH + par * 12288, 384, 384 },
-        };
-        gemv_run(J, cbase, 42, xs, red);
-      }
-      if (tid == 0) {
-        gate_arrive(bar, B_GRP, B_ROOT, B_GEN, g, 6, kb + 1);
-        waitgen(bar, B_GEN, kb + 2);
-      }
-      __syncthreads();
-    }
-  } else {
-    const int b = wg - 224;
-    for (int t = 0; t < 192; ++t) {
-      if (tid == 0) waitgen(bar, B_GEN, 2u * t + 2u);
-      __syncthreads();
-      per_b_predict(t, b, A, sm);
-      __syncthreads();
-      if (tid == 0)
-        __hip_atomic_fetch_add(bar + PRCNT, 1u, __ATOMIC_RELAXED, __HIP_MEMORY_SCOPE_AGENT);
-    }
-  }
+  const int lane = tid & 63;
+  const int wv = tid >> 6;
+  if (wg < 8)        l0_loop(wg * 4 + wv, lane, sm + wv * 384, A, bar);
+  else if (wg < 16)  l1_loop((wg - 8) * 4 + wv, lane, sm + wv * 384, A, bar);
+  else if (wg < 24)  pr_loop((wg - 16) * 4 + wv, lane, sm + wv * 384, A, bar);
+  else if (wg < 120) g0_loop(wg - 24, A, bar, sm);
+  else               g1_loop(wg - 120, A, bar, sm);
 }
 
 extern "C" void kernel_launch(void* const* d_in, const int* in_sizes, int n_in,
@@ -733,7 +781,7 @@
   k_conv<<<dim3(6, 96), 256, 0, stream>>>(ws + O_EMB, pconv1_w, pconv1_b, pbn_g, pbn_b, ws + O_H1);
   k_gate<<<6144, 256, 0, stream>>>(ws + O_H1, pconv2_w, pconv2_b, ws + O_GATEA, ws + O_GATEB);
   k_mg<<<24, 256, 0, stream>>>(ws + O_GATEA, ws + O_GATEB, ws + O_MG, ws + O_MGN);
-  k_zero<<<326, 256, 0, stream>>>(ws + O_P0S, (int)(O_DEADEND - O_P0S));
+  k_zero<<<328, 256, 0, stream>>>(ws + O_P0S, (int)(O_DEADEND - O_P0S));
   k_gemm<<<dim3(24, 96), 256, 0, stream>>>(ws + O_EMB, 384, r_wih, 384, r_bih,
                                            ws + O_IH0LN, 1536, 384, 0, nullptr, nullptr, nullptr);
   k_gemm<<<dim3(6, 96), 256, 0, stream>>>(ws + O_EMB, 384, r_proj_w, 768, r_proj_b,
@@ -741,7 +789,7 @@
   k_ln_rows<<<6144, 256, 0, stream>>>(ws + O_IH0LN, r_lnih_g, r_lnih_b);
   ScanArgs SA{ws, r_whh, r_bhh, r_lnhh_g, r_lnhh_b, r_lnih_g, r_lnih_b,
               r_lnc_g, r_lnc_b, r_wih, r_bih, r_proj_w, r_proj_b, p_proj_w, p_proj_b};
-  k_scan<<<256, 256, 0, stream>>>(SA);
+  k_scan<<<184, 256, 0, stream>>>(SA);
   k_gemm<<<dim3(6, 96), 256, 0, stream>>>(ws + O_OUTHS, 768, p_ffd_w, 768, p_ffd_b,
                                           nullptr, 384, 768, 1, p_bn_g, p_bn_b, out);
 }
```

Measured after the change: 13.02 ms. Within noise of the previous version (-1.0%).
